# Kernel optimization log

Hardware: AMD Instinct MI355X
Metric: run time of the kernel (lower is better)

## Reference

```python
import jax, jax.numpy as jnp
import numpy as np

B, ND, NE, D, H = 2, 2048, 2048, 1024, 16
HD = D // H
DFF = 4 * D
EPS = 1e-5


def setup_inputs() -> dict:
    key = jax.random.key(0)
    ks = jax.random.split(key, 16)
    s = lambda fan_in: 1.0 / np.sqrt(fan_in)
    inp = {
        'x': jax.random.normal(ks[0], (B, ND, D), jnp.float32),
        'memory': jax.random.normal(ks[1], (B, NE, D), jnp.float32),
        'ln1_g': jnp.ones((D,), jnp.float32), 'ln1_b': jnp.zeros((D,), jnp.float32),
        'Wqkv': jax.random.normal(ks[2], (D, 3 * D), jnp.float32) * s(D),
        'Wo_sa': jax.random.normal(ks[3], (D, D), jnp.float32) * s(D),
        'bo_sa': jnp.zeros((D,), jnp.float32),
        'ln2_g': jnp.ones((D,), jnp.float32), 'ln2_b': jnp.zeros((D,), jnp.float32),
        'Wq': jax.random.normal(ks[4], (D, D), jnp.float32) * s(D),
        'Wk': jax.random.normal(ks[5], (D, D), jnp.float32) * s(D),
        'Wv': jax.random.normal(ks[6], (D, D), jnp.float32) * s(D),
        'Wo_ca': jax.random.normal(ks[7], (D, D), jnp.float32) * s(D),
        'bo_ca': jnp.zeros((D,), jnp.float32),
        'ln3_g': jnp.ones((D,), jnp.float32), 'ln3_b': jnp.zeros((D,), jnp.float32),
        'W1': jax.random.normal(ks[8], (D, DFF), jnp.float32) * s(D),
        'b1': jnp.zeros((DFF,), jnp.float32),
        'W2': jax.random.normal(ks[9], (DFF, D), jnp.float32) * s(DFF),
        'b2': jnp.zeros((D,), jnp.float32),
        'attn_mask': jnp.tril(jnp.ones((ND, ND), jnp.bool_)),
    }
    return inp


def _layernorm(x, g, b):
    mu = jnp.mean(x, axis=-1, keepdims=True)
    var = jnp.mean(jnp.square(x - mu), axis=-1, keepdims=True)
    return (x - mu) * jax.lax.rsqrt(var + EPS) * g + b


def _heads(t, n):  # (B,N,D) -> (B,H,N,HD)
    Bn = t.shape[0]
    return t.reshape(Bn, n, H, HD).transpose(0, 2, 1, 3)


def _attend(q, k, v, mask=None):
    scale = HD ** -0.5
    scores = jnp.einsum('bhqd,bhkd->bhqk', q, k) * scale
    if mask is not None:
        scores = jnp.where(mask, scores, -jnp.inf)
    attn = jax.nn.softmax(scores, axis=-1)
    out = jnp.einsum('bhqk,bhkd->bhqd', attn, v)
    Bn, _, Nq, _ = out.shape
    return out.transpose(0, 2, 1, 3).reshape(Bn, Nq, D)


def reference(x, memory, ln1_g, ln1_b, Wqkv, Wo_sa, bo_sa, ln2_g, ln2_b,
              Wq, Wk, Wv, Wo_ca, bo_ca, ln3_g, ln3_b, W1, b1, W2, b2, attn_mask):
    # --- masked self-attention ---
    h = _layernorm(x, ln1_g, ln1_b)
    qkv = (h @ Wqkv).reshape(B, ND, 3, H, HD).transpose(2, 0, 3, 1, 4)  # (3,B,H,N,HD)
    q, k, v = qkv[0], qkv[1], qkv[2]
    sa = _attend(q, k, v, attn_mask[None, None]) @ Wo_sa + bo_sa
    x = x + sa
    # --- cross-attention ---
    h = _layernorm(x, ln2_g, ln2_b)
    q = _heads(h @ Wq, ND)
    k = _heads(memory @ Wk, NE)
    v = _heads(memory @ Wv, NE)
    ca = _attend(q, k, v) @ Wo_ca + bo_ca
    x = x + ca
    # --- FFN ---
    h = _layernorm(x, ln3_g, ln3_b)
    x = x + (jax.nn.gelu(h @ W1 + b1, approximate=False) @ W2 + b2)
    return x
```

## Files before the change

kernel.cpp:

```cpp
#include <hip/hip_runtime.h>
#include <hip/hip_bf16.h>
#include <math.h>

#define B_   2
#define ND_  2048
#define NE_  2048
#define D_   1024
#define H_   16
#define HD_  64
#define DFF_ 4096
#define T_   4096

typedef __attribute__((ext_vector_type(8))) short bf16x8;
typedef __attribute__((ext_vector_type(4))) float f32x4;

#if __has_builtin(__builtin_amdgcn_exp2f)
#define EXP2(x) __builtin_amdgcn_exp2f(x)
#else
#define EXP2(x) exp2f(x)
#endif

__device__ __forceinline__ short f2bf(float f) {
  union { float f; unsigned u; } v; v.f = f;
  return (short)((v.u + 0x7FFFu + ((v.u >> 16) & 1u)) >> 16);
}

typedef const __attribute__((address_space(1))) void gvoid_t;
typedef __attribute__((address_space(3))) void lvoid_t;

__device__ __forceinline__ void gload16(const void* src, void* dst) {
  __builtin_amdgcn_global_load_lds((gvoid_t*)src, (lvoid_t*)dst, 16, 0, 0);
}

__global__ __launch_bounds__(256) void wt_cast(const float* __restrict__ in,
                                               short* __restrict__ out,
                                               int K, int N) {
  __shared__ float t[32][33];
  const int tx = threadIdx.x, ty = threadIdx.y;
  const int n0 = blockIdx.x * 32, k0 = blockIdx.y * 32;
#pragma unroll
  for (int i = 0; i < 4; ++i)
    t[ty + i * 8][tx] = in[(size_t)(k0 + ty + i * 8) * N + n0 + tx];
  __syncthreads();
#pragma unroll
  for (int i = 0; i < 4; ++i)
    out[(size_t)(n0 + ty + i * 8) * K + k0 + tx] = f2bf(t[tx][ty + i * 8]);
}

__global__ __launch_bounds__(256) void castf2b(const float* __restrict__ in,
                                               short* __restrict__ out) {
  const int i = blockIdx.x * 256 + threadIdx.x;
  float4 v = ((const float4*)in)[i];
  short4 o;
  o.x = f2bf(v.x); o.y = f2bf(v.y); o.z = f2bf(v.z); o.w = f2bf(v.w);
  ((short4*)out)[i] = o;
}

__global__ __launch_bounds__(256) void ln_kernel(const float* __restrict__ x,
                                                 const float* __restrict__ g,
                                                 const float* __restrict__ b,
                                                 short* __restrict__ out) {
  const int row = blockIdx.x;
  const int tid = threadIdx.x;
  const float* xr = x + (size_t)row * D_;
  float4 v = reinterpret_cast<const float4*>(xr)[tid];
  float s  = v.x + v.y + v.z + v.w;
  float s2 = v.x * v.x + v.y * v.y + v.z * v.z + v.w * v.w;
#pragma unroll
  for (int m = 1; m < 64; m <<= 1) {
    s  += __shfl_xor(s, m);
    s2 += __shfl_xor(s2, m);
  }
  __shared__ float ss[4], ss2[4];
  const int w = tid >> 6;
  if ((tid & 63) == 0) { ss[w] = s; ss2[w] = s2; }
  __syncthreads();
  s  = ss[0] + ss[1] + ss[2] + ss[3];
  s2 = ss2[0] + ss2[1] + ss2[2] + ss2[3];
  const float mu   = s * (1.0f / D_);
  const float var  = s2 * (1.0f / D_) - mu * mu;
  const float rstd = rsqrtf(var + 1e-5f);
  float4 gv = reinterpret_cast<const float4*>(g)[tid];
  float4 bv = reinterpret_cast<const float4*>(b)[tid];
  short4 o;
  o.x = f2bf((v.x - mu) * rstd * gv.x + bv.x);
  o.y = f2bf((v.y - mu) * rstd * gv.y + bv.y);
  o.z = f2bf((v.z - mu) * rstd * gv.z + bv.z);
  o.w = f2bf((v.w - mu) * rstd * gv.w + bv.w);
  reinterpret_cast<short4*>(out + (size_t)row * D_)[tid] = o;
}

template <int MODE>
__global__ __launch_bounds__(256) void gemm_bt(const short* __restrict__ A,
                                               const short* __restrict__ Bt,
                                               const float* __restrict__ bias,
                                               const float* __restrict__ resid,
                                               void* __restrict__ Cout,
                                               int M, int N, int K) {
  __shared__ short As[128 * 32];
  __shared__ short Bs[128 * 32];
  const int tid = threadIdx.x;
  const int gx = gridDim.x;
  const int nwg = gx * gridDim.y;
  int lin = blockIdx.y * gx + blockIdx.x;
  lin = (lin & 7) * (nwg >> 3) + (lin >> 3);
  const int m0 = (lin / gx) * 128, n0 = (lin % gx) * 128;
  const int wave = tid >> 6, lane = tid & 63;
  const int wm = (wave >> 1) * 64, wn = (wave & 1) * 64;
  const int lr = lane & 15, lg = lane >> 4;

  f32x4 acc[4][4];
#pragma unroll
  for (int i = 0; i < 4; ++i)
#pragma unroll
    for (int j = 0; j < 4; ++j) acc[i][j] = f32x4{0.f, 0.f, 0.f, 0.f};

  const int e0 = tid * 8, e1 = 2048 + tid * 8;
  const int r0 = e0 >> 5, c0 = e0 & 31;
  const int r1 = e1 >> 5, c1 = e1 & 31;
  const size_t ar0 = (size_t)(m0 + r0) * K, ar1 = (size_t)(m0 + r1) * K;
  const size_t br0 = (size_t)(n0 + r0) * K, br1 = (size_t)(n0 + r1) * K;

  for (int k0 = 0; k0 < K; k0 += 32) {
    gload16(A + ar0 + k0 + c0, As + e0);
    gload16(A + ar1 + k0 + c1, As + e1);
    gload16(Bt + br0 + k0 + c0, Bs + e0);
    gload16(Bt + br1 + k0 + c1, Bs + e1);
    __syncthreads();
    bf16x8 af[4], bfr[4];
#pragma unroll
    for (int mi = 0; mi < 4; ++mi)
      af[mi] = *(const bf16x8*)(As + (wm + mi * 16 + lr) * 32 + lg * 8);
#pragma unroll
    for (int ni = 0; ni < 4; ++ni)
      bfr[ni] = *(const bf16x8*)(Bs + (wn + ni * 16 + lr) * 32 + lg * 8);
#pragma unroll
    for (int mi = 0; mi < 4; ++mi)
#pragma unroll
      for (int ni = 0; ni < 4; ++ni)
        acc[mi][ni] = __builtin_amdgcn_mfma_f32_16x16x32_bf16(
            af[mi], bfr[ni], acc[mi][ni], 0, 0, 0);
    __syncthreads();
  }

#pragma unroll
  for (int mi = 0; mi < 4; ++mi) {
    const int row = m0 + wm + mi * 16 + lg * 4;
#pragma unroll
    for (int ni = 0; ni < 4; ++ni) {
      const int col = n0 + wn + ni * 16 + lr;
#pragma unroll
      for (int r = 0; r < 4; ++r) {
        const size_t idx = (size_t)(row + r) * N + col;
        const float v = acc[mi][ni][r];
        if (MODE == 0) {
          ((short*)Cout)[idx] = f2bf(v);
        } else if (MODE == 1) {
          ((float*)Cout)[idx] = resid[idx] + v + bias[col];
        } else {
          const float tt = v + bias[col];
          const float yy = fmaf(tt * tt * tt, 0.044715f, tt);
          const float e = EXP2(yy * -2.3022343813918633f);
          ((short*)Cout)[idx] = f2bf(tt / (1.0f + e));
        }
      }
    }
  }
}

__global__ __launch_bounds__(256) void gemm_bt3(const short* __restrict__ A0,
                                                const short* __restrict__ A1,
                                                const short* __restrict__ A2,
                                                const short* __restrict__ B0,
                                                const short* __restrict__ B1,
                                                const short* __restrict__ B2,
                                                short* __restrict__ C0,
                                                short* __restrict__ C1,
                                                short* __restrict__ C2,
                                                int M, int N, int K) {
  const int z = blockIdx.z;
  const short* A  = z == 0 ? A0 : (z == 1 ? A1 : A2);
  const short* Bt = z == 0 ? B0 : (z == 1 ? B1 : B2);
  short* C        = z == 0 ? C0 : (z == 1 ? C1 : C2);

  __shared__ short As[128 * 32];
  __shared__ short Bs[128 * 32];
  const int tid = threadIdx.x;
  const int gx = gridDim.x;
  const int nwg = gx * gridDim.y;
  int lin = blockIdx.y * gx + blockIdx.x;
  lin = (lin & 7) * (nwg >> 3) + (lin >> 3);
  const int m0 = (lin / gx) * 128, n0 = (lin % gx) * 128;
  const int wave = tid >> 6, lane = tid & 63;
  const int wm = (wave >> 1) * 64, wn = (wave & 1) * 64;
  const int lr = lane & 15, lg = lane >> 4;

  f32x4 acc[4][4];
#pragma unroll
  for (int i = 0; i < 4; ++i)
#pragma unroll
    for (int j = 0; j < 4; ++j) acc[i][j] = f32x4{0.f, 0.f, 0.f, 0.f};

  const int e0 = tid * 8, e1 = 2048 + tid * 8;
  const int r0 = e0 >> 5, c0 = e0 & 31;
  const int r1 = e1 >> 5, c1 = e1 & 31;
  const size_t ar0 = (size_t)(m0 + r0) * K, ar1 = (size_t)(m0 + r1) * K;
  const size_t br0 = (size_t)(n0 + r0) * K, br1 = (size_t)(n0 + r1) * K;

  for (int k0 = 0; k0 < K; k0 += 32) {
    gload16(A + ar0 + k0 + c0, As + e0);
    gload16(A + ar1 + k0 + c1, As + e1);
    gload16(Bt + br0 + k0 + c0, Bs + e0);
    gload16(Bt + br1 + k0 + c1, Bs + e1);
    __syncthreads();
    bf16x8 af[4], bfr[4];
#pragma unroll
    for (int mi = 0; mi < 4; ++mi)
      af[mi] = *(const bf16x8*)(As + (wm + mi * 16 + lr) * 32 + lg * 8);
#pragma unroll
    for (int ni = 0; ni < 4; ++ni)
      bfr[ni] = *(const bf16x8*)(Bs + (wn + ni * 16 + lr) * 32 + lg * 8);
#pragma unroll
    for (int mi = 0; mi < 4; ++mi)
#pragma unroll
      for (int ni = 0; ni < 4; ++ni)
        acc[mi][ni] = __builtin_amdgcn_mfma_f32_16x16x32_bf16(
            af[mi], bfr[ni], acc[mi][ni], 0, 0, 0);
    __syncthreads();
  }

#pragma unroll
  for (int mi = 0; mi < 4; ++mi) {
    const int row = m0 + wm + mi * 16 + lg * 4;
#pragma unroll
    for (int ni = 0; ni < 4; ++ni) {
      const int col = n0 + wn + ni * 16 + lr;
#pragma unroll
      for (int r = 0; r < 4; ++r)
        C[(size_t)(row + r) * N + col] = f2bf(acc[mi][ni][r]);
    }
  }
}

__global__ __launch_bounds__(256) void gemm_bt64(const short* __restrict__ A,
                                                 const short* __restrict__ Bt,
                                                 const float* __restrict__ bias,
                                                 const float* __restrict__ resid,
                                                 float* __restrict__ Cout,
                                                 int M, int N, int K) {
  __shared__ short As[64 * 32];
  __shared__ short Bs[128 * 32];
  const int tid = threadIdx.x;
  const int gx = gridDim.x;
  const int nwg = gx * gridDim.y;
  int lin = blockIdx.y * gx + blockIdx.x;
  lin = (lin & 7) * (nwg >> 3) + (lin >> 3);
  const int m0 = (lin / gx) * 64, n0 = (lin % gx) * 128;
  const int wave = tid >> 6, lane = tid & 63;
  const int wn = wave * 32;
  const int lr = lane & 15, lg = lane >> 4;

  f32x4 acc[4][2];
#pragma unroll
  for (int i = 0; i < 4; ++i)
#pragma unroll
    for (int j = 0; j < 2; ++j) acc[i][j] = f32x4{0.f, 0.f, 0.f, 0.f};

  const int ea = tid * 8;
  const int ra = ea >> 5, ca = ea & 31;
  const int e0 = tid * 8, e1 = 2048 + tid * 8;
  const int r0 = e0 >> 5, c0 = e0 & 31;
  const int r1 = e1 >> 5, c1 = e1 & 31;
  const size_t ar = (size_t)(m0 + ra) * K;
  const size_t br0 = (size_t)(n0 + r0) * K, br1 = (size_t)(n0 + r1) * K;

  for (int k0 = 0; k0 < K; k0 += 32) {
    gload16(A + ar + k0 + ca, As + ea);
    gload16(Bt + br0 + k0 + c0, Bs + e0);
    gload16(Bt + br1 + k0 + c1, Bs + e1);
    __syncthreads();
    bf16x8 af[4], bfr[2];
#pragma unroll
    for (int mi = 0; mi < 4; ++mi)
      af[mi] = *(const bf16x8*)(As + (mi * 16 + lr) * 32 + lg * 8);
#pragma unroll
    for (int ni = 0; ni < 2; ++ni)
      bfr[ni] = *(const bf16x8*)(Bs + (wn + ni * 16 + lr) * 32 + lg * 8);
#pragma unroll
    for (int mi = 0; mi < 4; ++mi)
#pragma unroll
      for (int ni = 0; ni < 2; ++ni)
        acc[mi][ni] = __builtin_amdgcn_mfma_f32_16x16x32_bf16(
            af[mi], bfr[ni], acc[mi][ni], 0, 0, 0);
    __syncthreads();
  }

#pragma unroll
  for (int mi = 0; mi < 4; ++mi) {
    const int row = m0 + mi * 16 + lg * 4;
#pragma unroll
    for (int ni = 0; ni < 2; ++ni) {
      const int col = n0 + wn + ni * 16 + lr;
#pragma unroll
      for (int r = 0; r < 4; ++r) {
        const size_t idx = (size_t)(row + r) * N + col;
        Cout[idx] = resid[idx] + acc[mi][ni][r] + bias[col];
      }
    }
  }
}

__global__ __launch_bounds__(256) void vtrans(const short* __restrict__ in,
                                              short* __restrict__ out,
                                              int ldi, int N) {
  const int bh = blockIdx.z;
  const int b = bh >> 4, h = bh & 15;
  const short* ib = in + (size_t)b * N * ldi + h * HD_;
  short* ob = out + (size_t)bh * HD_ * N;
  __shared__ short t[32][33];
  const int tx = threadIdx.x, ty = threadIdx.y;
  const int n0 = blockIdx.x * 32, d0 = blockIdx.y * 32;
#pragma unroll
  for (int i = 0; i < 4; ++i)
    t[ty + i * 8][tx] = ib[(size_t)(n0 + ty + i * 8) * ldi + d0 + tx];
  __syncthreads();
#pragma unroll
  for (int i = 0; i < 4; ++i)
    ob[(size_t)(d0 + ty + i * 8) * N + n0 + tx] = t[tx][ty + i * 8];
}

__global__ __launch_bounds__(256) void flash(const short* __restrict__ Q,
                                             const short* __restrict__ Kp,
                                             const short* __restrict__ Vt,
                                             short* __restrict__ O,
                                             int ldq, int ldk, int ldo,
                                             int NK, int causal) {
  const int bh = blockIdx.x;
  int qb = blockIdx.y;
  if (causal) qb = (qb < 16) ? (2 * qb) : (63 - 2 * qb);
  const int b = bh >> 4, h = bh & 15;
  const int q0 = qb * 64;
  const int tid = threadIdx.x, wave = tid >> 6, lane = tid & 63;
  const int lr = lane & 15, lg = lane >> 4;
  const int lx = lr & 7;

  const short* Qb = Q + (size_t)b * ND_ * ldq + h * HD_;
  const short* Kb = Kp + (size_t)b * NK * ldk + h * HD_;
  const short* Vb = Vt + (size_t)bh * HD_ * NK;
  short* Ob = O + (size_t)b * ND_ * ldo + h * HD_;

  __shared__ short Ks[64 * 64];
  __shared__ short Vs[64 * 64];
  __shared__ short Ps[4][16 * 64];

  const int qrow = q0 + wave * 16 + lr;
  const bf16x8 qf0 = *(const bf16x8*)(Qb + (size_t)qrow * ldq + lg * 8);
  const bf16x8 qf1 = *(const bf16x8*)(Qb + (size_t)qrow * ldq + 32 + lg * 8);

  const bf16x8 ONES = {0x3F80, 0x3F80, 0x3F80, 0x3F80,
                       0x3F80, 0x3F80, 0x3F80, 0x3F80};

  f32x4 oacc[4];
  f32x4 lacc = f32x4{0.f, 0.f, 0.f, 0.f};
  float m_own = -1e30f;
#pragma unroll
  for (int i = 0; i < 4; ++i) oacc[i] = f32x4{0.f, 0.f, 0.f, 0.f};

  const int sr0 = tid >> 3;
  const int ssw = ((tid & 7) ^ (sr0 & 7)) * 8;
  const int e0 = tid * 8, e1 = 2048 + tid * 8;

  const float SC = 0.18033688011112042f;

  short* Pw = &Ps[wave][0];
  const int pbase = lr * 64 + (lg & 1) * 4;

  const int nkt = causal ? (qb + 1) : (NK / 64);
  for (int t = 0; t < nkt; ++t) {
    const int k0 = t * 64;
    gload16(Kb + (size_t)(k0 + sr0) * ldk + ssw, Ks + e0);
    gload16(Kb + (size_t)(k0 + 32 + sr0) * ldk + ssw, Ks + e1);
    gload16(Vb + (size_t)sr0 * NK + k0 + ssw, Vs + e0);
    gload16(Vb + (size_t)(32 + sr0) * NK + k0 + ssw, Vs + e1);
    __syncthreads();

    f32x4 st[4];
#pragma unroll
    for (int kb = 0; kb < 4; ++kb) {
      const bf16x8 kf0 = *(const bf16x8*)(Ks + (kb * 16 + lr) * 64 + ((lg ^ lx) * 8));
      const bf16x8 kf1 = *(const bf16x8*)(Ks + (kb * 16 + lr) * 64 + (((4 + lg) ^ lx) * 8));
      st[kb] = f32x4{0.f, 0.f, 0.f, 0.f};
      st[kb] = __builtin_amdgcn_mfma_f32_16x16x32_bf16(kf0, qf0, st[kb], 0, 0, 0);
      st[kb] = __builtin_amdgcn_mfma_f32_16x16x32_bf16(kf1, qf1, st[kb], 0, 0, 0);
    }
    if (causal && t == nkt - 1) {
#pragma unroll
      for (int kb = 0; kb < 4; ++kb)
#pragma unroll
        for (int r = 0; r < 4; ++r)
          if ((k0 + kb * 16 + lg * 4 + r) > qrow) st[kb][r] = -3.0e38f;
    }

    float rm = st[0][0];
#pragma unroll
    for (int kb = 0; kb < 4; ++kb)
#pragma unroll
      for (int r = 0; r < 4; ++r)
        if (kb || r) rm = fmaxf(rm, st[kb][r]);
    rm = fmaxf(rm, __shfl_xor(rm, 16));
    rm = fmaxf(rm, __shfl_xor(rm, 32));

    if (!__all(rm - m_own <= 44.f)) {
      const float nm = fmaxf(m_own, rm);
      const float fac = EXP2((m_own - nm) * SC);
      m_own = nm;
      const float fr0 = __shfl(fac, (lg << 2) + 0);
      const float fr1 = __shfl(fac, (lg << 2) + 1);
      const float fr2 = __shfl(fac, (lg << 2) + 2);
      const float fr3 = __shfl(fac, (lg << 2) + 3);
#pragma unroll
      for (int db = 0; db < 4; ++db) {
        oacc[db][0] *= fr0; oacc[db][1] *= fr1;
        oacc[db][2] *= fr2; oacc[db][3] *= fr3;
      }
      lacc[0] *= fr0; lacc[1] *= fr1; lacc[2] *= fr2; lacc[3] *= fr3;
    }
    const float nmsc = m_own * SC;
#pragma unroll
    for (int kb = 0; kb < 4; ++kb)
#pragma unroll
      for (int r = 0; r < 4; ++r)
        st[kb][r] = EXP2(fmaf(st[kb][r], SC, -nmsc));

#pragma unroll
    for (int kb = 0; kb < 4; ++kb) {
      const unsigned long long pk =
          (unsigned long long)(unsigned short)f2bf(st[kb][0]) |
          ((unsigned long long)(unsigned short)f2bf(st[kb][1]) << 16) |
          ((unsigned long long)(unsigned short)f2bf(st[kb][2]) << 32) |
          ((unsigned long long)(unsigned short)f2bf(st[kb][3]) << 48);
      const int cs = kb * 2 + (lg >> 1);
      *(unsigned long long*)(Pw + pbase + ((cs ^ lx) * 8)) = pk;
    }
    const bf16x8 pf0 = *(const bf16x8*)(Pw + lr * 64 + ((lg ^ lx) * 8));
    const bf16x8 pf1 = *(const bf16x8*)(Pw + lr * 64 + (((4 + lg) ^ lx) * 8));

#pragma unroll
    for (int db = 0; db < 4; ++db) {
      const bf16x8 vf0 = *(const bf16x8*)(Vs + (db * 16 + lr) * 64 + ((lg ^ lx) * 8));
      const bf16x8 vf1 = *(const bf16x8*)(Vs + (db * 16 + lr) * 64 + (((4 + lg) ^ lx) * 8));
      oacc[db] = __builtin_amdgcn_mfma_f32_16x16x32_bf16(pf0, vf0, oacc[db], 0, 0, 0);
      oacc[db] = __builtin_amdgcn_mfma_f32_16x16x32_bf16(pf1, vf1, oacc[db], 0, 0, 0);
    }
    lacc = __builtin_amdgcn_mfma_f32_16x16x32_bf16(pf0, ONES, lacc, 0, 0, 0);
    lacc = __builtin_amdgcn_mfma_f32_16x16x32_bf16(pf1, ONES, lacc, 0, 0, 0);
    __syncthreads();
  }
#pragma unroll
  for (int db = 0; db < 4; ++db)
#pragma unroll
    for (int r = 0; r < 4; ++r) {
      const int q = q0 + wave * 16 + lg * 4 + r;
      Ob[(size_t)q * ldo + db * 16 + lr] = f2bf(oacc[db][r] / lacc[r]);
    }
}

extern "C" void kernel_launch(void* const* d_in, const int* in_sizes, int n_in,
                              void* d_out, int out_size, void* d_ws, size_t ws_size,
                              hipStream_t stream) {
  const float* x      = (const float*)d_in[0];
  const float* memory = (const float*)d_in[1];
  const float* ln1_g  = (const float*)d_in[2];
  const float* ln1_b  = (const float*)d_in[3];
  const float* Wqkv   = (const float*)d_in[4];
  const float* Wo_sa  = (const float*)d_in[5];
  const float* bo_sa  = (const float*)d_in[6];
  const float* ln2_g  = (const float*)d_in[7];
  const float* ln2_b  = (const float*)d_in[8];
  const float* Wq     = (const float*)d_in[9];
  const float* Wk     = (const float*)d_in[10];
  const float* Wv     = (const float*)d_in[11];
  const float* Wo_ca  = (const float*)d_in[12];
  const float* bo_ca  = (const float*)d_in[13];
  const float* ln3_g  = (const float*)d_in[14];
  const float* ln3_b  = (const float*)d_in[15];
  const float* W1     = (const float*)d_in[16];
  const float* b1     = (const float*)d_in[17];
  const float* W2     = (const float*)d_in[18];
  const float* b2     = (const float*)d_in[19];

  char* ws = (char*)d_ws;
  size_t o = 0;
  auto alloc = [&](size_t bytes) { char* p = ws + o; o += bytes; return p; };
  short* wqkv_t = (short*)alloc((size_t)3072 * 1024 * 2);
  short* wosa_t = (short*)alloc((size_t)1024 * 1024 * 2);
  short* wq_t   = (short*)alloc((size_t)1024 * 1024 * 2);
  short* wk_t   = (short*)alloc((size_t)1024 * 1024 * 2);
  short* wv_t   = (short*)alloc((size_t)1024 * 1024 * 2);
  short* woca_t = (short*)alloc((size_t)1024 * 1024 * 2);
  short* w1_t   = (short*)alloc((size_t)4096 * 1024 * 2);
  short* w2_t   = (short*)alloc((size_t)1024 * 4096 * 2);
  short* hbf    = (short*)alloc((size_t)T_ * 1024 * 2);
  short* bufa   = (short*)alloc((size_t)T_ * 3072 * 2);
  short* vt     = (short*)alloc((size_t)32 * 64 * 2048 * 2);
  short* attn   = (short*)alloc((size_t)T_ * 1024 * 2);
  short* membf  = (short*)alloc((size_t)T_ * 1024 * 2);
  float* x1     = (float*)alloc((size_t)T_ * 1024 * 4);
  float* x2     = (float*)alloc((size_t)T_ * 1024 * 4);
  if (o > ws_size) return;

  short* ffn = bufa;
  short* qca = bufa;
  short* kca = bufa + (size_t)T_ * 1024;
  short* vca = bufa + (size_t)2 * T_ * 1024;

  const dim3 tb(32, 8);

  wt_cast<<<dim3(3072 / 32, 1024 / 32), tb, 0, stream>>>(Wqkv, wqkv_t, 1024, 3072);
  wt_cast<<<dim3(1024 / 32, 1024 / 32), tb, 0, stream>>>(Wo_sa, wosa_t, 1024, 1024);
  wt_cast<<<dim3(1024 / 32, 1024 / 32), tb, 0, stream>>>(Wq, wq_t, 1024, 1024);
  wt_cast<<<dim3(1024 / 32, 1024 / 32), tb, 0, stream>>>(Wk, wk_t, 1024, 1024);
  wt_cast<<<dim3(1024 / 32, 1024 / 32), tb, 0, stream>>>(Wv, wv_t, 1024, 1024);
  wt_cast<<<dim3(1024 / 32, 1024 / 32), tb, 0, stream>>>(Wo_ca, woca_t, 1024, 1024);
  wt_cast<<<dim3(4096 / 32, 1024 / 32), tb, 0, stream>>>(W1, w1_t, 1024, 4096);
  wt_cast<<<dim3(1024 / 32, 4096 / 32), tb, 0, stream>>>(W2, w2_t, 4096, 1024);
  castf2b<<<dim3((T_ * 1024) / (256 * 4)), 256, 0, stream>>>(memory, membf);

  ln_kernel<<<dim3(T_), 256, 0, stream>>>(x, ln1_g, ln1_b, hbf);
  gemm_bt<0><<<dim3(3072 / 128, T_ / 128), 256, 0, stream>>>(
      hbf, wqkv_t, nullptr, nullptr, bufa, T_, 3072, 1024);
  vtrans<<<dim3(ND_ / 32, HD_ / 32, 32), tb, 0, stream>>>(bufa + 2048, vt, 3072, ND_);
  flash<<<dim3(32, ND_ / 64), 256, 0, stream>>>(
      bufa, bufa + 1024, vt, attn, 3072, 3072, 1024, ND_, 1);
  gemm_bt64<<<dim3(1024 / 128, T_ / 64), 256, 0, stream>>>(
      attn, wosa_t, bo_sa, x, x1, T_, 1024, 1024);

  ln_kernel<<<dim3(T_), 256, 0, stream>>>(x1, ln2_g, ln2_b, hbf);
  gemm_bt3<<<dim3(1024 / 128, T_ / 128, 3), 256, 0, stream>>>(
      hbf, membf, membf, wq_t, wk_t, wv_t, qca, kca, vca, T_, 1024, 1024);
  vtrans<<<dim3(NE_ / 32, HD_ / 32, 32), tb, 0, stream>>>(vca, vt, 1024, NE_);
  flash<<<dim3(32, ND_ / 64), 256, 0, stream>>>(
      qca, kca, vt, attn, 1024, 1024, 1024, NE_, 0);
  gemm_bt64<<<dim3(1024 / 128, T_ / 64), 256, 0, stream>>>(
      attn, woca_t, bo_ca, x1, x2, T_, 1024, 1024);

  ln_kernel<<<dim3(T_), 256, 0, stream>>>(x2, ln3_g, ln3_b, hbf);
  gemm_bt<2><<<dim3(4096 / 128, T_ / 128), 256, 0, stream>>>(
      hbf, w1_t, b1, nullptr, ffn, T_, 4096, 1024);
  gemm_bt64<<<dim3(1024 / 128, T_ / 64), 256, 0, stream>>>(
      ffn, w2_t, b2, x2, (float*)d_out, T_, 1024, 4096);
}
```

Before: 427.0 us.

## Move residual+bias into LayerNorm kernels, store projection outputs as bf16

The output-projection GEMMs now write bf16 deltas instead of fp32 residual sums, and new ln_fused kernels add residual, bias and delta before normalizing. A final addbias kernel handles the last residual. Five square weight casts are batched into one launch, and the flash P packing uses v_cvt_pk_bf16_f32. This cuts fp32 traffic in the GEMM epilogues and launch count, but rounds the residual delta to bf16 (a precision loss) and adds a kernel at the end. ln_fused reads delta from hbf and writes its LN output back to hbf in place.

Result: no change. 421.1 us (-1.4%).

```diff
diff --git a/kernel.cpp b/kernel.cpp
--- a/kernel.cpp
+++ b/kernel.cpp
@@ -24,6 +24,10 @@
   union { float f; unsigned u; } v; v.f = f;
   return (short)((v.u + 0x7FFFu + ((v.u >> 16) & 1u)) >> 16);
 }
+__device__ __forceinline__ float bf2f(short s) {
+  union { unsigned u; float f; } v; v.u = ((unsigned)(unsigned short)s) << 16;
+  return v.f;
+}
 
 typedef const __attribute__((address_space(1))) void gvoid_t;
 typedef __attribute__((address_space(3))) void lvoid_t;
@@ -45,6 +49,31 @@
 #pragma unroll
   for (int i = 0; i < 4; ++i)
     out[(size_t)(n0 + ty + i * 8) * K + k0 + tx] = f2bf(t[tx][ty + i * 8]);
+}
+
+__global__ __launch_bounds__(256) void wt_cast5(const float* __restrict__ i0,
+                                                const float* __restrict__ i1,
+                                                const float* __restrict__ i2,
+                                                const float* __restrict__ i3,
+                                                const float* __restrict__ i4,
+                                                short* __restrict__ o0,
+                                                short* __restrict__ o1,
+                                                short* __restrict__ o2,
+                                                short* __restrict__ o3,
+                                                short* __restrict__ o4) {
+  const int z = blockIdx.z;
+  const float* in = z == 0 ? i0 : z == 1 ? i1 : z == 2 ? i2 : z == 3 ? i3 : i4;
+  short* out      = z == 0 ? o0 : z == 1 ? o1 : z == 2 ? o2 : z == 3 ? o3 : o4;
+  __shared__ float t[32][33];
+  const int tx = threadIdx.x, ty = threadIdx.y;
+  const int n0 = blockIdx.x * 32, k0 = blockIdx.y * 32;
+#pragma unroll
+  for (int i = 0; i < 4; ++i)
+    t[ty + i * 8][tx] = in[(size_t)(k0 + ty + i * 8) * 1024 + n0 + tx];
+  __syncthreads();
+#pragma unroll
+  for (int i = 0; i < 4; ++i)
+    out[(size_t)(n0 + ty + i * 8) * 1024 + k0 + tx] = f2bf(t[tx][ty + i * 8]);
 }
 
 __global__ __launch_bounds__(256) void castf2b(const float* __restrict__ in,
@@ -90,11 +119,69 @@
   reinterpret_cast<short4*>(out + (size_t)row * D_)[tid] = o;
 }
 
+__global__ __launch_bounds__(256) void ln_fused(const float* __restrict__ xprev,
+                                                const short* delta,
+                                                const float* __restrict__ pbias,
+                                                const float* __restrict__ g,
+                                                const float* __restrict__ b,
+                                                short* out_ln,
+                                                float* __restrict__ out_x) {
+  const int row = blockIdx.x;
+  const int tid = threadIdx.x;
+  float4 v = reinterpret_cast<const float4*>(xprev + (size_t)row * D_)[tid];
+  short4 dv = reinterpret_cast<const short4*>(delta + (size_t)row * D_)[tid];
+  float4 pb = reinterpret_cast<const float4*>(pbias)[tid];
+  v.x += bf2f(dv.x) + pb.x;
+  v.y += bf2f(dv.y) + pb.y;
+  v.z += bf2f(dv.z) + pb.z;
+  v.w += bf2f(dv.w) + pb.w;
+  float s  = v.x + v.y + v.z + v.w;
+  float s2 = v.x * v.x + v.y * v.y + v.z * v.z + v.w * v.w;
+#pragma unroll
+  for (int m = 1; m < 64; m <<= 1) {
+    s  += __shfl_xor(s, m);
+    s2 += __shfl_xor(s2, m);
+  }
+  __shared__ float ss[4], ss2[4];
+  const int w = tid >> 6;
+  if ((tid & 63) == 0) { ss[w] = s; ss2[w] = s2; }
+  __syncthreads();
+  s  = ss[0] + ss[1] + ss[2] + ss[3];
+  s2 = ss2[0] + ss2[1] + ss2[2] + ss2[3];
+  const float mu   = s * (1.0f / D_);
+  const float var  = s2 * (1.0f / D_) - mu * mu;
+  const float rstd = rsqrtf(var + 1e-5f);
+  reinterpret_cast<float4*>(out_x + (size_t)row * D_)[tid] = v;
+  float4 gv = reinterpret_cast<const float4*>(g)[tid];
+  float4 bv = reinterpret_cast<const float4*>(b)[tid];
+  short4 o;
+  o.x = f2bf((v.x - mu) * rstd * gv.x + bv.x);
+  o.y = f2bf((v.y - mu) * rstd * gv.y + bv.y);
+  o.z = f2bf((v.z - mu) * rstd * gv.z + bv.z);
+  o.w = f2bf((v.w - mu) * rstd * gv.w + bv.w);
+  reinterpret_cast<short4*>(out_ln + (size_t)row * D_)[tid] = o;
+}
+
+__global__ __launch_bounds__(256) void addbias(const float* __restrict__ x,
+                                               const short* __restrict__ delta,
+                                               const float* __restrict__ bias,
+                                               float* __restrict__ out) {
+  const int i = blockIdx.x * 256 + threadIdx.x;
+  float4 v = ((const float4*)x)[i];
+  short4 dv = ((const short4*)delta)[i];
+  const int col = (i * 4) & (D_ - 1);
+  float4 pb = *(const float4*)(bias + col);
+  v.x += bf2f(dv.x) + pb.x;
+  v.y += bf2f(dv.y) + pb.y;
+  v.z += bf2f(dv.z) + pb.z;
+  v.w += bf2f(dv.w) + pb.w;
+  ((float4*)out)[i] = v;
+}
+
 template <int MODE>
 __global__ __launch_bounds__(256) void gemm_bt(const short* __restrict__ A,
                                                const short* __restrict__ Bt,
                                                const float* __restrict__ bias,
-                                               const float* __restrict__ resid,
                                                void* __restrict__ Cout,
                                                int M, int N, int K) {
   __shared__ short As[128 * 32];
@@ -155,8 +242,6 @@
         const float v = acc[mi][ni][r];
         if (MODE == 0) {
           ((short*)Cout)[idx] = f2bf(v);
-        } else if (MODE == 1) {
-          ((float*)Cout)[idx] = resid[idx] + v + bias[col];
         } else {
           const float tt = v + bias[col];
           const float yy = fmaf(tt * tt * tt, 0.044715f, tt);
@@ -244,9 +329,7 @@
 
 __global__ __launch_bounds__(256) void gemm_bt64(const short* __restrict__ A,
                                                  const short* __restrict__ Bt,
-                                                 const float* __restrict__ bias,
-                                                 const float* __restrict__ resid,
-                                                 float* __restrict__ Cout,
+                                                 short* __restrict__ Cout,
                                                  int M, int N, int K) {
   __shared__ short As[64 * 32];
   __shared__ short Bs[128 * 32];
@@ -302,10 +385,8 @@
     for (int ni = 0; ni < 2; ++ni) {
       const int col = n0 + wn + ni * 16 + lr;
 #pragma unroll
-      for (int r = 0; r < 4; ++r) {
-        const size_t idx = (size_t)(row + r) * N + col;
-        Cout[idx] = resid[idx] + acc[mi][ni][r] + bias[col];
-      }
+      for (int r = 0; r < 4; ++r)
+        Cout[(size_t)(row + r) * N + col] = f2bf(acc[mi][ni][r]);
     }
   }
 }
@@ -434,13 +515,13 @@
 
 #pragma unroll
     for (int kb = 0; kb < 4; ++kb) {
-      const unsigned long long pk =
-          (unsigned long long)(unsigned short)f2bf(st[kb][0]) |
-          ((unsigned long long)(unsigned short)f2bf(st[kb][1]) << 16) |
-          ((unsigned long long)(unsigned short)f2bf(st[kb][2]) << 32) |
-          ((unsigned long long)(unsigned short)f2bf(st[kb][3]) << 48);
+      union { unsigned u[2]; unsigned long long ull; } pk;
+      asm("v_cvt_pk_bf16_f32 %0, %1, %2"
+          : "=v"(pk.u[0]) : "v"(st[kb][0]), "v"(st[kb][1]));
+      asm("v_cvt_pk_bf16_f32 %0, %1, %2"
+          : "=v"(pk.u[1]) : "v"(st[kb][2]), "v"(st[kb][3]));
       const int cs = kb * 2 + (lg >> 1);
-      *(unsigned long long*)(Pw + pbase + ((cs ^ lx) * 8)) = pk;
+      *(unsigned long long*)(Pw + pbase + ((cs ^ lx) * 8)) = pk.ull;
     }
     const bf16x8 pf0 = *(const bf16x8*)(Pw + lr * 64 + ((lg ^ lx) * 8));
     const bf16x8 pf1 = *(const bf16x8*)(Pw + lr * 64 + (((4 + lg) ^ lx) * 8));
@@ -517,36 +598,35 @@
   const dim3 tb(32, 8);
 
   wt_cast<<<dim3(3072 / 32, 1024 / 32), tb, 0, stream>>>(Wqkv, wqkv_t, 1024, 3072);
-  wt_cast<<<dim3(1024 / 32, 1024 / 32), tb, 0, stream>>>(Wo_sa, wosa_t, 1024, 1024);
-  wt_cast<<<dim3(1024 / 32, 1024 / 32), tb, 0, stream>>>(Wq, wq_t, 1024, 1024);
-  wt_cast<<<dim3(1024 / 32, 1024 / 32), tb, 0, stream>>>(Wk, wk_t, 1024, 1024);
-  wt_cast<<<dim3(1024 / 32, 1024 / 32), tb, 0, stream>>>(Wv, wv_t, 1024, 1024);
-  wt_cast<<<dim3(1024 / 32, 1024 / 32), tb, 0, stream>>>(Wo_ca, woca_t, 1024, 1024);
+  wt_cast5<<<dim3(32, 32, 5), tb, 0, stream>>>(Wo_sa, Wq, Wk, Wv, Wo_ca,
+                                               wosa_t, wq_t, wk_t, wv_t, woca_t);
   wt_cast<<<dim3(4096 / 32, 1024 / 32), tb, 0, stream>>>(W1, w1_t, 1024, 4096);
   wt_cast<<<dim3(1024 / 32, 4096 / 32), tb, 0, stream>>>(W2, w2_t, 4096, 1024);
   castf2b<<<dim3((T_ * 1024) / (256 * 4)), 256, 0, stream>>>(memory, membf);
 
   ln_kernel<<<dim3(T_), 256, 0, stream>>>(x, ln1_g, ln1_b, hbf);
   gemm_bt<0><<<dim3(3072 / 128, T_ / 128), 256, 0, stream>>>(
-      hbf, wqkv_t, nullptr, nullptr, bufa, T_, 3072, 1024);
+      hbf, wqkv_t, nullptr, bufa, T_, 3072, 1024);
   vtrans<<<dim3(ND_ / 32, HD_ / 32, 32), tb, 0, stream>>>(bufa + 2048, vt, 3072, ND_);
   flash<<<dim3(32, ND_ / 64), 256, 0, stream>>>(
       bufa, bufa + 1024, vt, attn, 3072, 3072, 1024, ND_, 1);
   gemm_bt64<<<dim3(1024 / 128, T_ / 64), 256, 0, stream>>>(
-      attn, wosa_t, bo_sa, x, x1, T_, 1024, 1024);
-
-  ln_kernel<<<dim3(T_), 256, 0, stream>>>(x1, ln2_g, ln2_b, hbf);
+      attn, wosa_t, hbf, T_, 1024, 1024);
+  ln_fused<<<dim3(T_), 256, 0, stream>>>(x, hbf, bo_sa, ln2_g, ln2_b, hbf, x1);
+
   gemm_bt3<<<dim3(1024 / 128, T_ / 128, 3), 256, 0, stream>>>(
       hbf, membf, membf, wq_t, wk_t, wv_t, qca, kca, vca, T_, 1024, 1024);
   vtrans<<<dim3(NE_ / 32, HD_ / 32, 32), tb, 0, stream>>>(vca, vt, 1024, NE_);
   flash<<<dim3(32, ND_ / 64), 256, 0, stream>>>(
       qca, kca, vt, attn, 1024, 1024, 1024, NE_, 0);
   gemm_bt64<<<dim3(1024 / 128, T_ / 64), 256, 0, stream>>>(
-      attn, woca_t, bo_ca, x1, x2, T_, 1024, 1024);
-
-  ln_kernel<<<dim3(T_), 256, 0, stream>>>(x2, ln3_g, ln3_b, hbf);
+      attn, woca_t, hbf, T_, 1024, 1024);
+  ln_fused<<<dim3(T_), 256, 0, stream>>>(x1, hbf, bo_ca, ln3_g, ln3_b, hbf, x2);
+
   gemm_bt<2><<<dim3(4096 / 128, T_ / 128), 256, 0, stream>>>(
-      hbf, w1_t, b1, nullptr, ffn, T_, 4096, 1024);
+      hbf, w1_t, b1, ffn, T_, 4096, 1024);
   gemm_bt64<<<dim3(1024 / 128, T_ / 64), 256, 0, stream>>>(
-      ffn, w2_t, b2, x2, (float*)d_out, T_, 1024, 4096);
-}
+      ffn, w2_t, hbf, T_, 1024, 4096);
+  addbias<<<dim3((T_ * 1024) / (256 * 4)), 256, 0, stream>>>(
+      x2, hbf, b2, (float*)d_out);
+}
```
